# Kernel optimization log

Hardware: AMD Instinct MI355X
Metric: run time of the kernel (lower is better)

Reference implementation:

```python
import jax, jax.numpy as jnp
import numpy as np

NUM_HEADS = 8
CODEBOOK_SIZE = 1024
HEAD_DIM = 128
BATCH = 32768


def setup_inputs() -> dict:
    key = jax.random.key(0)
    k_z, k_cb = jax.random.split(key)
    z = jax.random.normal(k_z, (BATCH, NUM_HEADS * HEAD_DIM), dtype=jnp.float32)
    codebooks = jax.random.normal(k_cb, (NUM_HEADS, CODEBOOK_SIZE, HEAD_DIM), dtype=jnp.float32)
    return {"z": z, "codebooks": codebooks}


def reference(z, codebooks):
    # z: [B, H*D]; codebooks: [H, K, D]
    H, K, D = codebooks.shape
    B = z.shape[0]
    zh = z.reshape(B, H, D)
    # Squared euclidean distances ||z - c||^2 = ||z||^2 - 2 z.c + ||c||^2.
    # torch.cdist(p=2) applies sqrt, but sqrt is monotone so argmin is identical.
    z_sq = jnp.sum(zh * zh, axis=-1)                       # [B, H]
    c_sq = jnp.sum(codebooks * codebooks, axis=-1)         # [H, K]
    cross = jnp.einsum('bhd,hkd->bhk', zh, codebooks)      # [B, H, K]
    d2 = z_sq[:, :, None] - 2.0 * cross + c_sq[None, :, :]  # [B, H, K]
    idx = jnp.argmin(d2, axis=-1)                          # [B, H] int
    # Gather nearest codes per head: codebooks[h, idx[b,h]] -> [B, H, D]
    zq = codebooks[jnp.arange(H)[None, :], idx]
    # Straight-through estimator: forward = codes, backward = identity on z.
    zq = zh + jax.lax.stop_gradient(zq - zh)
    return zq.reshape(B, H * D), idx
```

## Files before the change

### kernel.cpp

```cpp
#include <hip/hip_runtime.h>

namespace {
constexpr int kNH = 8;
constexpr int kK  = 1024;
constexpr int kD  = 128;
constexpr int kB  = 32768;

constexpr int BM  = 128;
constexpr int kMarginQ = 4;
constexpr float kMarginF32 = 0.0625f;

constexpr size_t kOffCsq  = 4096;
constexpr size_t kOffCbF  = 65536;
constexpr size_t kOffPart = 65536 + 4194304;
constexpr size_t kOffWl6  = 65536 + 8388608;
constexpr size_t kOffWl5  = 65536 + 4194304;
}

typedef short           bf16x8 __attribute__((ext_vector_type(8)));
typedef unsigned short  us16x8 __attribute__((ext_vector_type(8)));
typedef float           f32x16 __attribute__((ext_vector_type(16)));

__device__ __forceinline__ unsigned short f2bf_rne(float f) {
    unsigned int x = __float_as_uint(f);
    unsigned int r = (x + 0x7fffu + ((x >> 16) & 1u)) >> 16;
    return (unsigned short)r;
}
__device__ __forceinline__ float bf2f(unsigned short u) {
    return __uint_as_float(((unsigned int)u) << 16);
}

__global__ void pq_prep(const float* __restrict__ cb,
                        unsigned short* __restrict__ cbf,
                        float* __restrict__ csq)
{
    int code = blockIdx.x;
    int t = threadIdx.x;
    int h = code >> 10, k = code & 1023;
    int kt = k >> 6, cv = (k >> 5) & 1, l31 = k & 31;
    int kc = t >> 4, hh = (t >> 3) & 1, j = t & 7;
    float v = cb[(size_t)code * kD + t];
    unsigned short hb = f2bf_rne(v);
    unsigned short lb = f2bf_rne(v - bf2f(hb));
    size_t base = ((((size_t)h * 16 + kt) * 8 + kc) * 2 + cv) * 2048;
    size_t off  = base + (hh * 32 + l31) * 16 + j * 2;
    *(unsigned short*)((char*)cbf + off)        = hb;
    *(unsigned short*)((char*)cbf + off + 1024) = lb;
    __shared__ double red[128];
    red[t] = (double)v * (double)v;
    __syncthreads();
    for (int s = 64; s > 0; s >>= 1) {
        if (t < s) red[t] += red[t + s];
        __syncthreads();
    }
    if (t == 0) csq[code] = (float)(red[0] * 1024.0);
}

__global__ __launch_bounds__(512, 2)
void pq_coarse_mfma4(const float* __restrict__ z,
                     const unsigned short* __restrict__ cbf,
                     const float* __restrict__ csq1024,
                     int2* __restrict__ part)
{
    __shared__ unsigned short zbuf[2][2][32 * kD];
    __shared__ int2 P[2][8][32];

    const int t    = threadIdx.x;
    const int lane = t & 63;
    const int w    = t >> 6;
    const int l31  = lane & 31, h32 = lane >> 5;
    const int h    = blockIdx.y;
    const int half = blockIdx.z;
    const int rb0  = blockIdx.x * 1024;

    bf16x8 Ah[8][2], Al[8][2];
    {
        const char* base = (const char*)cbf
            + (((size_t)h * 16 + half * 8 + w) * 16) * 2048 + lane * 16;
        #pragma unroll
        for (int kc = 0; kc < 8; ++kc)
            #pragma unroll
            for (int cv = 0; cv < 2; ++cv) {
                const char* p = base + (size_t)(kc * 2 + cv) * 2048;
                Ah[kc][cv] = *(const bf16x8*)p;
                Al[kc][cv] = *(const bf16x8*)(p + 1024);
            }
    }
    float csel[2][16];
    {
        const float* cs = csq1024 + h * kK + half * 512 + w * 64 + h32 * 4;
        #pragma unroll
        for (int cv = 0; cv < 2; ++cv)
            #pragma unroll
            for (int r = 0; r < 16; ++r)
                csel[cv][r] = cs[cv * 32 + (r & 3) + ((r >> 2) << 3)];
    }

    float4 zA, zB;
    auto issueZ = [&](int tile) {
        const float* zp = z + (size_t)(rb0 + tile * 32 + (t >> 4)) * (kNH * kD)
                            + h * kD + (t & 15) * 8;
        zA = *(const float4*)zp;
        zB = *(const float4*)(zp + 4);
    };
    auto commitZ = [&](int buf) {
        float f[8] = {zA.x, zA.y, zA.z, zA.w, zB.x, zB.y, zB.z, zB.w};
        us16x8 hv, lv;
        #pragma unroll
        for (int j = 0; j < 8; ++j) {
            unsigned short hb = f2bf_rne(f[j]);
            hv[j] = hb;
            lv[j] = f2bf_rne(f[j] - bf2f(hb));
        }
        int r = t >> 4, seg = t & 15;
        int off = r * 256 + ((seg * 16) ^ ((r & 15) << 4));
        *(us16x8*)((char*)&zbuf[buf][0][0] + off) = hv;
        *(us16x8*)((char*)&zbuf[buf][1][0] + off) = lv;
    };
    auto mergeP = [&](int pb, int tile) {
        int2 m = P[pb][0][t];
        int m1 = m.x, m2 = m.y;
        #pragma unroll
        for (int ww = 1; ww < 8; ++ww) {
            int2 p = P[pb][ww][t];
            int mx = max(m1, p.x);
            m1 = min(m1, p.x);
            m2 = min(min(m2, p.y), mx);
        }
        int gid = (rb0 + tile * 32 + t) * kNH + h;
        part[(size_t)gid * 2 + half] = make_int2(m1, m2);
    };

    issueZ(0);
    commitZ(0);
    __syncthreads();

    int cur = 0;
    const int cgb = half * 512 + w * 64 + h32 * 4;
    for (int tile = 0; tile < 32; ++tile) {
        if (tile + 1 < 32) issueZ(tile + 1);
        if (tile > 0 && t < 32) mergeP(cur ^ 1, tile - 1);

        f32x16 acc0 = (f32x16)0.0f, acc1 = (f32x16)0.0f;
        const char* zh0 = (const char*)&zbuf[cur][0][0];
        const char* zl0 = (const char*)&zbuf[cur][1][0];
        const int boff = l31 * 256;
        const int swz  = (l31 & 15) << 4;
        #pragma unroll
        for (int kc = 0; kc < 8; ++kc) {
            int col = (kc * 32 + h32 * 16) ^ swz;
            bf16x8 Bh = *(const bf16x8*)(zh0 + boff + col);
            bf16x8 Bl = *(const bf16x8*)(zl0 + boff + col);
            __builtin_amdgcn_s_setprio(1);
            acc0 = __builtin_amdgcn_mfma_f32_32x32x16_bf16(Ah[kc][0], Bh, acc0, 0, 0, 0);
            acc1 = __builtin_amdgcn_mfma_f32_32x32x16_bf16(Ah[kc][1], Bh, acc1, 0, 0, 0);
            acc0 = __builtin_amdgcn_mfma_f32_32x32x16_bf16(Al[kc][0], Bh, acc0, 0, 0, 0);
            acc1 = __builtin_amdgcn_mfma_f32_32x32x16_bf16(Al[kc][1], Bh, acc1, 0, 0, 0);
            acc0 = __builtin_amdgcn_mfma_f32_32x32x16_bf16(Ah[kc][0], Bl, acc0, 0, 0, 0);
            acc1 = __builtin_amdgcn_mfma_f32_32x32x16_bf16(Ah[kc][1], Bl, acc1, 0, 0, 0);
            __builtin_amdgcn_s_setprio(0);
        }
        int b1 = 0x7fffffff, b2 = 0x7fffffff;
        #pragma unroll
        for (int r = 0; r < 16; ++r) {
            int cr = (r & 3) + ((r >> 2) << 3);
            {
                float kf = fmaf(acc0[r], -2048.0f, csel[0][r]);
                int key = ((int)kf << 10) + cgb + cr;
                int mx = max(b1, key); b1 = min(b1, key); b2 = min(b2, mx);
            }
            {
                float kf = fmaf(acc1[r], -2048.0f, csel[1][r]);
                int key = ((int)kf << 10) + cgb + cr + 32;
                int mx = max(b1, key); b1 = min(b1, key); b2 = min(b2, mx);
            }
        }
        int o1 = __shfl_xor(b1, 32), o2 = __shfl_xor(b2, 32);
        int mx2 = max(b1, o1);
        int v1 = min(b1, o1);
        int v2 = min(min(b2, o2), mx2);
        if (h32 == 0) P[cur][w][l31] = make_int2(v1, v2);

        if (tile + 1 < 32) commitZ(cur ^ 1);
        __syncthreads();
        cur ^= 1;
    }
    if (t < 32) mergeP(cur ^ 1, 31);
}

__global__ __launch_bounds__(256)
void pq_merge(const int2* __restrict__ part, const float* __restrict__ cb,
              float* __restrict__ out_zq, float* __restrict__ out_idx,
              unsigned int* wl_count, unsigned int* wl, unsigned int wl_cap)
{
    __shared__ int idx_s[128];
    const int t = threadIdx.x;
    const int g0 = blockIdx.x * 128;
    if (t < 128) {
        int gid = g0 + t;
        int2 p0 = part[(size_t)gid * 2];
        int2 p1 = part[(size_t)gid * 2 + 1];
        int mx = max(p0.x, p1.x);
        int v1 = min(p0.x, p1.x);
        int v2 = min(min(p0.y, p1.y), mx);
        int idx = v1 & 1023;
        idx_s[t] = idx;
        out_idx[gid] = (float)idx;
        if (wl_cap > 0u && ((v2 >> 10) - (v1 >> 10)) <= kMarginQ) {
            unsigned int pos = atomicAdd(wl_count, 1u);
            if (pos < wl_cap) wl[pos] = (unsigned int)gid;
        }
    }
    __syncthreads();
    #pragma unroll
    for (int it = 0; it < 16; ++it) {
        int c = it * 256 + t;
        int row = c >> 5, c4 = c & 31;
        int gid = g0 + row;
        int b = gid >> 3, hh = gid & 7;
        *(float4*)(out_zq + (size_t)b * (kNH * kD) + hh * kD + c4 * 4) =
            *(const float4*)(cb + ((size_t)hh * kK + idx_s[row]) * kD + c4 * 4);
    }
}

__global__ __launch_bounds__(256, 2)
void pq_coarse_mfma3(const float* __restrict__ z, const float* __restrict__ cb,
                     const unsigned short* __restrict__ cbf,
                     const float* __restrict__ csq1024,
                     float* __restrict__ out_zq, float* __restrict__ out_idx,
                     unsigned int* wl_count, unsigned int* wl, unsigned int wl_cap)
{
    __shared__ float csq_s[kK];
    __shared__ int   idx_s[BM];

    const int t    = threadIdx.x;
    const int h    = blockIdx.y;
    const int b0   = blockIdx.x * BM;
    const int lane = t & 63;
    const int w    = t >> 6;
    const int l31  = lane & 31, h32 = lane >> 5;

    *(float4*)&csq_s[t * 4] = *(const float4*)(csq1024 + h * kK + t * 4);

    bf16x8 Ah[8], Al[8];
    {
        const float* zr = z + (size_t)(b0 + w * 32 + l31) * (kNH * kD) + h * kD + h32 * 8;
        #pragma unroll
        for (int kc = 0; kc < 8; ++kc) {
            float4 a = *(const float4*)(zr + kc * 16);
            float4 b = *(const float4*)(zr + kc * 16 + 4);
            float f[8] = {a.x, a.y, a.z, a.w, b.x, b.y, b.z, b.w};
            bf16x8 hv, lv;
            #pragma unroll
            for (int j = 0; j < 8; ++j) {
                unsigned short hb = f2bf_rne(f[j]);
                hv[j] = (short)hb;
                lv[j] = (short)f2bf_rne(f[j] - bf2f(hb));
            }
            Ah[kc] = hv;
            Al[kc] = lv;
        }
    }
    __syncthreads();

    int b1[16], b2[16];
    #pragma unroll
    for (int r = 0; r < 16; ++r) { b1[r] = 0x7fffffff; b2[r] = 0x7fffffff; }

    const char* bbase = (const char*)cbf + (size_t)h * 524288 + lane * 16;
#define LDSLOT(kt_, kc_, s_)                                                  \
    {                                                                         \
        const char* p_ = bbase + (size_t)(((kt_) * 8 + (kc_)) * 2) * 2048;    \
        Bh0[s_] = *(const bf16x8*)(p_);                                       \
        Bl0[s_] = *(const bf16x8*)(p_ + 1024);                                \
        Bh1[s_] = *(const bf16x8*)(p_ + 2048);                                \
        Bl1[s_] = *(const bf16x8*)(p_ + 3072);                                \
    }

    bf16x8 Bh0[4], Bl0[4], Bh1[4], Bl1[4];
    LDSLOT(0, 0, 0);
    LDSLOT(0, 1, 1);

    for (int kt = 0; kt < 16; ++kt) {
        f32x16 acc0 = (f32x16)0.0f, acc1 = (f32x16)0.0f;
        const int ktn = (kt + 1 < 16) ? kt + 1 : kt;
        #pragma unroll
        for (int kc = 0; kc < 8; ++kc) {
            const int s  = kc & 3;
            const int s2 = (kc + 2) & 3;
            if (kc < 6) { LDSLOT(kt, kc + 2, s2); } else { LDSLOT(ktn, kc - 6, s2); }
            __builtin_amdgcn_s_setprio(1);
            acc0 = __builtin_amdgcn_mfma_f32_32x32x16_bf16(Ah[kc], Bh0[s], acc0, 0, 0, 0);
            acc1 = __builtin_amdgcn_mfma_f32_32x32x16_bf16(Ah[kc], Bh1[s], acc1, 0, 0, 0);
            acc0 = __builtin_amdgcn_mfma_f32_32x32x16_bf16(Al[kc], Bh0[s], acc0, 0, 0, 0);
            acc1 = __builtin_amdgcn_mfma_f32_32x32x16_bf16(Al[kc], Bh1[s], acc1, 0, 0, 0);
            acc0 = __builtin_amdgcn_mfma_f32_32x32x16_bf16(Ah[kc], Bl0[s], acc0, 0, 0, 0);
            acc1 = __builtin_amdgcn_mfma_f32_32x32x16_bf16(Ah[kc], Bl1[s], acc1, 0, 0, 0);
            __builtin_amdgcn_s_setprio(0);
        }
        const float cs0 = csq_s[kt * 64 + l31];
        const float cs1 = csq_s[kt * 64 + 32 + l31];
        const int   kg0 = kt * 64 + l31, kg1 = kg0 + 32;
        #pragma unroll
        for (int r = 0; r < 16; ++r) {
            {
                float kf = fmaf(acc0[r], -2048.0f, cs0);
                int key = ((int)kf << 10) + kg0;
                int mx = max(b1[r], key); b1[r] = min(b1[r], key); b2[r] = min(b2[r], mx);
            }
            {
                float kf = fmaf(acc1[r], -2048.0f, cs1);
                int key = ((int)kf << 10) + kg1;
                int mx = max(b1[r], key); b1[r] = min(b1[r], key); b2[r] = min(b2[r], mx);
            }
        }
    }
#undef LDSLOT

    #pragma unroll
    for (int r = 0; r < 16; ++r) {
        int v1 = b1[r], v2 = b2[r];
        #pragma unroll
        for (int m = 1; m < 32; m <<= 1) {
            int o1 = __shfl_xor(v1, m);
            int o2 = __shfl_xor(v2, m);
            int mx = max(v1, o1);
            v1 = min(v1, o1);
            v2 = min(min(v2, o2), mx);
        }
        if (l31 == 0) {
            int row = w * 32 + (r & 3) + ((r >> 2) << 3) + h32 * 4;
            int idx = v1 & 1023;
            idx_s[row] = idx;
            int gid = (b0 + row) * kNH + h;
            out_idx[gid] = (float)idx;
            if (wl_cap > 0u && ((v2 >> 10) - (v1 >> 10)) <= kMarginQ) {
                unsigned int pos = atomicAdd(wl_count, 1u);
                if (pos < wl_cap) wl[pos] = (unsigned int)gid;
            }
        }
    }
    __syncthreads();
    {
        const float* cbh_row = cb + (size_t)h * kK * kD;
        #pragma unroll
        for (int it = 0; it < 16; ++it) {
            int c = it * 256 + t;
            int row = c >> 5, col4 = c & 31;
            *(float4*)(out_zq + (size_t)(b0 + row) * (kNH * kD) + h * kD + col4 * 4) =
                *(const float4*)(cbh_row + (size_t)idx_s[row] * kD + col4 * 4);
        }
    }
}

__global__ __launch_bounds__(256, 2)
void pq_coarse_f32(const float* __restrict__ z, const float* __restrict__ cb,
                   float* __restrict__ out_zq, float* __restrict__ out_idx,
                   unsigned int* wl_count, unsigned int* wl, unsigned int wl_cap)
{
    constexpr int KT = 64, PAD = 68, BMF = 64;
    __shared__ float zT[kD][PAD];
    __shared__ float cT[kD][PAD];
    __shared__ float csq_s[KT];
    __shared__ int   bidx_s[BMF];

    const int t  = threadIdx.x;
    const int h  = blockIdx.y;
    const int b0 = blockIdx.x * BMF;
    const int tx = t & 15, ty = t >> 4;
    const int r8 = t & 7,  d4 = t >> 3;

    {
        const float* zp = z + (size_t)(b0 + r8) * (kNH * kD) + h * kD + 4 * d4;
        #pragma unroll
        for (int it = 0; it < BMF / 8; ++it) {
            float4 v = *(const float4*)(zp + (size_t)(8 * it) * (kNH * kD));
            int r = r8 + 8 * it;
            zT[4 * d4 + 0][r] = v.x; zT[4 * d4 + 1][r] = v.y;
            zT[4 * d4 + 2][r] = v.z; zT[4 * d4 + 3][r] = v.w;
        }
    }
    float best1[4], best2[4]; int ibest[4];
    #pragma unroll
    for (int i = 0; i < 4; ++i) { best1[i] = 3.4e38f; best2[i] = 3.4e38f; ibest[i] = 0; }

    for (int kt = 0; kt < kK / KT; ++kt) {
        __syncthreads();
        {
            const float* cp = cb + ((size_t)h * kK + kt * KT + r8) * kD + 4 * d4;
            #pragma unroll
            for (int it = 0; it < KT / 8; ++it) {
                float4 v = *(const float4*)(cp + (size_t)(8 * it) * kD);
                int r = r8 + 8 * it;
                cT[4 * d4 + 0][r] = v.x; cT[4 * d4 + 1][r] = v.y;
                cT[4 * d4 + 2][r] = v.z; cT[4 * d4 + 3][r] = v.w;
            }
        }
        if (t < KT) csq_s[t] = 0.0f;
        __syncthreads();
        {
            int kk = t & 63, part = t >> 6;
            float s = 0.f;
            #pragma unroll
            for (int i = 0; i < 32; ++i) { float v = cT[32 * part + i][kk]; s = fmaf(v, v, s); }
            atomicAdd(&csq_s[kk], s);
        }
        __syncthreads();
        float accA[4][4] = {{0}}, accB[4][4] = {{0}};
        #pragma unroll 2
        for (int d = 0; d < kD; d += 2) {
            float4 za = *(const float4*)&zT[d][4 * ty];
            float4 ca = *(const float4*)&cT[d][4 * tx];
            float4 zb = *(const float4*)&zT[d + 1][4 * ty];
            float4 cv = *(const float4*)&cT[d + 1][4 * tx];
            float zav[4] = {za.x, za.y, za.z, za.w}, cav[4] = {ca.x, ca.y, ca.z, ca.w};
            float zbv[4] = {zb.x, zb.y, zb.z, zb.w}, cbv[4] = {cv.x, cv.y, cv.z, cv.w};
            #pragma unroll
            for (int i = 0; i < 4; ++i)
                #pragma unroll
                for (int j = 0; j < 4; ++j) {
                    accA[i][j] = fmaf(zav[i], cav[j], accA[i][j]);
                    accB[i][j] = fmaf(zbv[i], cbv[j], accB[i][j]);
                }
        }
        #pragma unroll
        for (int j = 0; j < 4; ++j) {
            int kk = 4 * tx + j;
            float cs = csq_s[kk];
            int kg = kt * KT + kk;
            #pragma unroll
            for (int i = 0; i < 4; ++i) {
                float s = fmaf(-2.0f, accA[i][j] + accB[i][j], cs);
                if (s < best1[i]) { best2[i] = best1[i]; best1[i] = s; ibest[i] = kg; }
                else if (s < best2[i]) { best2[i] = s; }
            }
        }
    }
    __syncthreads();
    float* redv1 = &zT[0][0];
    float* redv2 = redv1 + BMF * 16;
    int*   redi  = (int*)(redv2 + BMF * 16);
    #pragma unroll
    for (int i = 0; i < 4; ++i) {
        int r = 4 * ty + i;
        redv1[r * 16 + tx] = best1[i]; redv2[r * 16 + tx] = best2[i]; redi[r * 16 + tx] = ibest[i];
    }
    __syncthreads();
    if (t < BMF) {
        int r = t;
        float vb1_ = redv1[r * 16], vb2_ = redv2[r * 16];
        int i1 = redi[r * 16];
        #pragma unroll
        for (int x = 1; x < 16; ++x) {
            float nb1 = redv1[r * 16 + x], nb2 = redv2[r * 16 + x];
            int ni1 = redi[r * 16 + x];
            if (nb1 < vb1_ || (nb1 == vb1_ && ni1 < i1)) { vb2_ = fminf(vb1_, nb2); vb1_ = nb1; i1 = ni1; }
            else vb2_ = fminf(vb2_, nb1);
        }
        bidx_s[r] = i1;
        int gid = (b0 + r) * kNH + h;
        out_idx[gid] = (float)i1;
        if (wl_cap > 0u && (vb2_ - vb1_) <= kMarginF32) {
            unsigned int pos = atomicAdd(wl_count, 1u);
            if (pos < wl_cap) wl[pos] = (unsigned int)gid;
        }
    }
    __syncthreads();
    {
        int r = t >> 2, q = t & 3;
        const float* src = cb + ((size_t)h * kK + bidx_s[r]) * kD;
        float* dst = out_zq + (size_t)(b0 + r) * (kNH * kD) + h * kD;
        #pragma unroll
        for (int m = 0; m < 8; ++m) {
            int jj = 4 * m + q;
            *(float4*)(dst + 4 * jj) = *(const float4*)(src + 4 * jj);
        }
    }
}

__global__ __launch_bounds__(256)
void pq_exact(const float* __restrict__ z, const float* __restrict__ cb,
              float* __restrict__ out_zq, float* __restrict__ out_idx,
              const unsigned int* wl_count, const unsigned int* wl,
              unsigned int wl_cap)
{
    if (wl_cap == 0u) return;
    __shared__ float  zs[kD];
    __shared__ double rv[256];
    __shared__ int    ri[256];
    unsigned int n = *wl_count;
    if (n > wl_cap) n = wl_cap;
    const int t = threadIdx.x;
    for (unsigned int e = blockIdx.x; e < n; e += gridDim.x) {
        unsigned int id = wl[e];
        int b = (int)(id / kNH), h = (int)(id % kNH);
        if (t < kD) zs[t] = z[(size_t)b * (kNH * kD) + h * kD + t];
        __syncthreads();
        double bv = 1e300; int bi = 0;
        #pragma unroll
        for (int kk = 0; kk < 4; ++kk) {
            int k = t * 4 + kk;
            const float* c = cb + ((size_t)h * kK + k) * kD;
            double s = 0.0;
            for (int d = 0; d < kD; ++d) {
                double diff = (double)zs[d] - (double)c[d];
                s = fma(diff, diff, s);
            }
            if (s < bv) { bv = s; bi = k; }
        }
        rv[t] = bv; ri[t] = bi;
        __syncthreads();
        for (int s2 = 128; s2 > 0; s2 >>= 1) {
            if (t < s2) {
                if (rv[t + s2] < rv[t] || (rv[t + s2] == rv[t] && ri[t + s2] < ri[t])) {
                    rv[t] = rv[t + s2]; ri[t] = ri[t + s2];
                }
            }
            __syncthreads();
        }
        int kbest = ri[0];
        if (t == 0) out_idx[id] = (float)kbest;
        if (t < kD)
            out_zq[(size_t)b * (kNH * kD) + h * kD + t] =
                cb[((size_t)h * kK + kbest) * kD + t];
        __syncthreads();
    }
}

extern "C" void kernel_launch(void* const* d_in, const int* in_sizes, int n_in,
                              void* d_out, int out_size, void* d_ws, size_t ws_size,
                              hipStream_t stream)
{
    const float* z  = (const float*)d_in[0];
    const float* cb = (const float*)d_in[1];
    float* out_zq  = (float*)d_out;
    float* out_idx = out_zq + (size_t)kB * kNH * kD;
    char* ws = (char*)d_ws;

    if (ws_size >= kOffWl6 + 65536) {
        unsigned int* wl_count = (unsigned int*)ws;
        unsigned int* wl = (unsigned int*)(ws + kOffWl6);
        size_t c = (ws_size - kOffWl6) / 4;
        unsigned int cap = (unsigned int)(c > 262144 ? 262144 : c);
        float* csq = (float*)(ws + kOffCsq);
        unsigned short* cbf = (unsigned short*)(ws + kOffCbF);
        int2* part = (int2*)(ws + kOffPart);

        hipMemsetAsync(d_ws, 0, 4, stream);
        pq_prep<<<kNH * kK, kD, 0, stream>>>(cb, cbf, csq);
        dim3 grid(32, kNH, 2);
        pq_coarse_mfma4<<<grid, 512, 0, stream>>>(z, cbf, csq, part);
        pq_merge<<<kB * kNH / 128, 256, 0, stream>>>(part, cb, out_zq, out_idx,
                                                     wl_count, wl, cap);
        pq_exact<<<256, 256, 0, stream>>>(z, cb, out_zq, out_idx, wl_count, wl, cap);
    } else if (ws_size >= kOffWl5 + 4096) {
        unsigned int* wl_count = (unsigned int*)ws;
        unsigned int* wl = (unsigned int*)(ws + kOffWl5);
        size_t c = (ws_size - kOffWl5) / 4;
        unsigned int cap = (unsigned int)(c > 262144 ? 262144 : c);
        float* csq = (float*)(ws + kOffCsq);
        unsigned short* cbf = (unsigned short*)(ws + kOffCbF);

        hipMemsetAsync(d_ws, 0, 4, stream);
        pq_prep<<<kNH * kK, kD, 0, stream>>>(cb, cbf, csq);
        dim3 grid(kB / BM, kNH);
        pq_coarse_mfma3<<<grid, 256, 0, stream>>>(z, cb, cbf, csq,
                                                  out_zq, out_idx, wl_count, wl, cap);
        pq_exact<<<256, 256, 0, stream>>>(z, cb, out_zq, out_idx, wl_count, wl, cap);
    } else {
        unsigned int* wl_count = (unsigned int*)ws;
        unsigned int* wl = wl_count + 1;
        unsigned int cap = 0;
        if (ws_size >= 64) {
            size_t c = ws_size / 4 - 1;
            cap = (unsigned int)(c > 262144 ? 262144 : c);
            hipMemsetAsync(d_ws, 0, 4, stream);
        }
        dim3 grid(kB / 64, kNH);
        pq_coarse_f32<<<grid, 256, 0, stream>>>(z, cb, out_zq, out_idx, wl_count, wl, cap);
        pq_exact<<<256, 256, 0, stream>>>(z, cb, out_zq, out_idx, wl_count, wl, cap);
    }
}
```

Baseline: 238.4 us.

## Stream codebook fragments from global and double the per-phase row tile

The coarse MFMA kernel no longer holds the whole codebook slice in registers. It streams A fragments from global memory through a two-slot register ring, one K-chunk ahead. Each phase now processes 64 z rows instead of 32, so every loaded A fragment feeds twice as many MFMAs. The change also packs bf16 with a cheaper bias-and-perm conversion, keeps the top-2 running minimum with v_med3, and rotates the merge work across waves. Register pressure drops, but codebook reloads now hit L2/global on every phase, and the kernel depends on that latency being hidden behind the MFMAs.

Measured after the change: 320.8 us. 1.35x slower.

```diff
diff --git a/kernel.cpp b/kernel.cpp
--- a/kernel.cpp
+++ b/kernel.cpp
@@ -28,6 +28,11 @@
 }
 __device__ __forceinline__ float bf2f(unsigned short u) {
     return __uint_as_float(((unsigned int)u) << 16);
+}
+__device__ __forceinline__ int med3_i32(int a, int b, int c) {
+    int d;
+    asm("v_med3_i32 %0, %1, %2, %3" : "=v"(d) : "v"(a), "v"(b), "v"(c));
+    return d;
 }
 
 __global__ void pq_prep(const float* __restrict__ cb,
@@ -57,13 +62,13 @@
 }
 
 __global__ __launch_bounds__(512, 2)
-void pq_coarse_mfma4(const float* __restrict__ z,
+void pq_coarse_mfma5(const float* __restrict__ z,
                      const unsigned short* __restrict__ cbf,
                      const float* __restrict__ csq1024,
                      int2* __restrict__ part)
 {
-    __shared__ unsigned short zbuf[2][2][32 * kD];
-    __shared__ int2 P[2][8][32];
+    __shared__ unsigned short zbuf[2][2][64 * kD];
+    __shared__ int2 P[2][8][64];
 
     const int t    = threadIdx.x;
     const int lane = t & 63;
@@ -73,119 +78,156 @@
     const int half = blockIdx.z;
     const int rb0  = blockIdx.x * 1024;
 
-    bf16x8 Ah[8][2], Al[8][2];
-    {
-        const char* base = (const char*)cbf
-            + (((size_t)h * 16 + half * 8 + w) * 16) * 2048 + lane * 16;
-        #pragma unroll
-        for (int kc = 0; kc < 8; ++kc)
-            #pragma unroll
-            for (int cv = 0; cv < 2; ++cv) {
-                const char* p = base + (size_t)(kc * 2 + cv) * 2048;
-                Ah[kc][cv] = *(const bf16x8*)p;
-                Al[kc][cv] = *(const bf16x8*)(p + 1024);
-            }
-    }
-    float csel[2][16];
+    const char* pb = (const char*)cbf
+        + (size_t)((h * 16 + half * 8 + w) * 16) * 2048 + lane * 16;
+
+    float csel0[16], csel1[16];
     {
         const float* cs = csq1024 + h * kK + half * 512 + w * 64 + h32 * 4;
         #pragma unroll
-        for (int cv = 0; cv < 2; ++cv)
-            #pragma unroll
-            for (int r = 0; r < 16; ++r)
-                csel[cv][r] = cs[cv * 32 + (r & 3) + ((r >> 2) << 3)];
-    }
-
-    float4 zA, zB;
-    auto issueZ = [&](int tile) {
-        const float* zp = z + (size_t)(rb0 + tile * 32 + (t >> 4)) * (kNH * kD)
-                            + h * kD + (t & 15) * 8;
-        zA = *(const float4*)zp;
-        zB = *(const float4*)(zp + 4);
+        for (int r = 0; r < 16; ++r) {
+            int cr = (r & 3) + ((r >> 2) << 3);
+            csel0[r] = cs[cr];
+            csel1[r] = cs[32 + cr];
+        }
+    }
+    const int cgb = half * 512 + w * 64 + h32 * 4;
+
+    float4 pA, pB, pC, pD;
+    auto issueZ = [&](int phase) {
+        const float* zp = z + (size_t)(rb0 + phase * 64 + (t >> 5)) * (kNH * kD)
+                            + h * kD + (t & 31) * 4;
+        pA = *(const float4*)zp;
+        pB = *(const float4*)(zp + 16 * (kNH * kD));
+        pC = *(const float4*)(zp + 32 * (kNH * kD));
+        pD = *(const float4*)(zp + 48 * (kNH * kD));
+    };
+    auto commit1 = [&](int buf, int rowq, float4 v) {
+        unsigned bx = __float_as_uint(v.x) + 0x8000u;
+        unsigned by = __float_as_uint(v.y) + 0x8000u;
+        unsigned bz = __float_as_uint(v.z) + 0x8000u;
+        unsigned bw = __float_as_uint(v.w) + 0x8000u;
+        unsigned h01 = __builtin_amdgcn_perm(by, bx, 0x07060302u);
+        unsigned h23 = __builtin_amdgcn_perm(bw, bz, 0x07060302u);
+        float rx = v.x - __uint_as_float(bx & 0xffff0000u);
+        float ry = v.y - __uint_as_float(by & 0xffff0000u);
+        float rz = v.z - __uint_as_float(bz & 0xffff0000u);
+        float rw = v.w - __uint_as_float(bw & 0xffff0000u);
+        unsigned l01 = __builtin_amdgcn_perm(__float_as_uint(ry) + 0x8000u,
+                                             __float_as_uint(rx) + 0x8000u, 0x07060302u);
+        unsigned l23 = __builtin_amdgcn_perm(__float_as_uint(rw) + 0x8000u,
+                                             __float_as_uint(rz) + 0x8000u, 0x07060302u);
+        int col4 = t & 31;
+        int off = rowq * 256 + (((col4 >> 1) * 16) ^ ((rowq & 15) << 4)) + (col4 & 1) * 8;
+        uint2 hv = {h01, h23}, lv = {l01, l23};
+        *(uint2*)((char*)&zbuf[buf][0][0] + off) = hv;
+        *(uint2*)((char*)&zbuf[buf][1][0] + off) = lv;
     };
     auto commitZ = [&](int buf) {
-        float f[8] = {zA.x, zA.y, zA.z, zA.w, zB.x, zB.y, zB.z, zB.w};
-        us16x8 hv, lv;
-        #pragma unroll
-        for (int j = 0; j < 8; ++j) {
-            unsigned short hb = f2bf_rne(f[j]);
-            hv[j] = hb;
-            lv[j] = f2bf_rne(f[j] - bf2f(hb));
-        }
-        int r = t >> 4, seg = t & 15;
-        int off = r * 256 + ((seg * 16) ^ ((r & 15) << 4));
-        *(us16x8*)((char*)&zbuf[buf][0][0] + off) = hv;
-        *(us16x8*)((char*)&zbuf[buf][1][0] + off) = lv;
+        commit1(buf,  0 + (t >> 5), pA);
+        commit1(buf, 16 + (t >> 5), pB);
+        commit1(buf, 32 + (t >> 5), pC);
+        commit1(buf, 48 + (t >> 5), pD);
     };
-    auto mergeP = [&](int pb, int tile) {
-        int2 m = P[pb][0][t];
+    auto mergeP = [&](int pbuf, int phase) {
+        int2 m = P[pbuf][0][lane];
         int m1 = m.x, m2 = m.y;
         #pragma unroll
         for (int ww = 1; ww < 8; ++ww) {
-            int2 p = P[pb][ww][t];
+            int2 p = P[pbuf][ww][lane];
             int mx = max(m1, p.x);
             m1 = min(m1, p.x);
             m2 = min(min(m2, p.y), mx);
         }
-        int gid = (rb0 + tile * 32 + t) * kNH + h;
+        int gid = (rb0 + phase * 64 + lane) * kNH + h;
         part[(size_t)gid * 2 + half] = make_int2(m1, m2);
     };
 
+    bf16x8 sAh[2][2], sAl[2][2];
+#define LOADSLOT(kc_, s_)                                                     \
+    {                                                                         \
+        const char* q0 = pb + (size_t)((kc_) * 2 + 0) * 2048;                 \
+        const char* q1 = pb + (size_t)((kc_) * 2 + 1) * 2048;                 \
+        sAh[s_][0] = *(const bf16x8*)q0;                                      \
+        sAl[s_][0] = *(const bf16x8*)(q0 + 1024);                             \
+        sAh[s_][1] = *(const bf16x8*)q1;                                      \
+        sAl[s_][1] = *(const bf16x8*)(q1 + 1024);                             \
+    }
+
     issueZ(0);
     commitZ(0);
-    __syncthreads();
-
+    LOADSLOT(0, 0);
+    __syncthreads();
+
+    const int swz = (l31 & 15) << 4;
     int cur = 0;
-    const int cgb = half * 512 + w * 64 + h32 * 4;
-    for (int tile = 0; tile < 32; ++tile) {
-        if (tile + 1 < 32) issueZ(tile + 1);
-        if (tile > 0 && t < 32) mergeP(cur ^ 1, tile - 1);
-
-        f32x16 acc0 = (f32x16)0.0f, acc1 = (f32x16)0.0f;
+    for (int phase = 0; phase < 16; ++phase) {
+        if (phase + 1 < 16) issueZ(phase + 1);
+        if (phase > 0 && w == ((phase - 1) & 7)) mergeP(cur ^ 1, phase - 1);
+
+        f32x16 a00 = (f32x16)0.0f, a01 = (f32x16)0.0f;
+        f32x16 a10 = (f32x16)0.0f, a11 = (f32x16)0.0f;
         const char* zh0 = (const char*)&zbuf[cur][0][0];
         const char* zl0 = (const char*)&zbuf[cur][1][0];
-        const int boff = l31 * 256;
-        const int swz  = (l31 & 15) << 4;
         #pragma unroll
         for (int kc = 0; kc < 8; ++kc) {
-            int col = (kc * 32 + h32 * 16) ^ swz;
-            bf16x8 Bh = *(const bf16x8*)(zh0 + boff + col);
-            bf16x8 Bl = *(const bf16x8*)(zl0 + boff + col);
+            const int sl = kc & 1;
+            if (kc < 7) { LOADSLOT(kc + 1, ((kc + 1) & 1)); }
+            else        { LOADSLOT(0, 0); }
+            const int col = (kc * 32 + h32 * 16) ^ swz;
+            bf16x8 B0h = *(const bf16x8*)(zh0 + l31 * 256 + col);
+            bf16x8 B0l = *(const bf16x8*)(zl0 + l31 * 256 + col);
+            bf16x8 B1h = *(const bf16x8*)(zh0 + (32 + l31) * 256 + col);
+            bf16x8 B1l = *(const bf16x8*)(zl0 + (32 + l31) * 256 + col);
             __builtin_amdgcn_s_setprio(1);
-            acc0 = __builtin_amdgcn_mfma_f32_32x32x16_bf16(Ah[kc][0], Bh, acc0, 0, 0, 0);
-            acc1 = __builtin_amdgcn_mfma_f32_32x32x16_bf16(Ah[kc][1], Bh, acc1, 0, 0, 0);
-            acc0 = __builtin_amdgcn_mfma_f32_32x32x16_bf16(Al[kc][0], Bh, acc0, 0, 0, 0);
-            acc1 = __builtin_amdgcn_mfma_f32_32x32x16_bf16(Al[kc][1], Bh, acc1, 0, 0, 0);
-            acc0 = __builtin_amdgcn_mfma_f32_32x32x16_bf16(Ah[kc][0], Bl, acc0, 0, 0, 0);
-            acc1 = __builtin_amdgcn_mfma_f32_32x32x16_bf16(Ah[kc][1], Bl, acc1, 0, 0, 0);
+            a00 = __builtin_amdgcn_mfma_f32_32x32x16_bf16(sAh[sl][0], B0h, a00, 0, 0, 0);
+            a01 = __builtin_amdgcn_mfma_f32_32x32x16_bf16(sAh[sl][0], B1h, a01, 0, 0, 0);
+            a10 = __builtin_amdgcn_mfma_f32_32x32x16_bf16(sAh[sl][1], B0h, a10, 0, 0, 0);
+            a11 = __builtin_amdgcn_mfma_f32_32x32x16_bf16(sAh[sl][1], B1h, a11, 0, 0, 0);
+            a00 = __builtin_amdgcn_mfma_f32_32x32x16_bf16(sAl[sl][0], B0h, a00, 0, 0, 0);
+            a01 = __builtin_amdgcn_mfma_f32_32x32x16_bf16(sAl[sl][0], B1h, a01, 0, 0, 0);
+            a10 = __builtin_amdgcn_mfma_f32_32x32x16_bf16(sAl[sl][1], B0h, a10, 0, 0, 0);
+            a11 = __builtin_amdgcn_mfma_f32_32x32x16_bf16(sAl[sl][1], B1h, a11, 0, 0, 0);
+            a00 = __builtin_amdgcn_mfma_f32_32x32x16_bf16(sAh[sl][0], B0l, a00, 0, 0, 0);
+            a01 = __builtin_amdgcn_mfma_f32_32x32x16_bf16(sAh[sl][0], B1l, a01, 0, 0, 0);
+            a10 = __builtin_amdgcn_mfma_f32_32x32x16_bf16(sAh[sl][1], B0l, a10, 0, 0, 0);
+            a11 = __builtin_amdgcn_mfma_f32_32x32x16_bf16(sAh[sl][1], B1l, a11, 0, 0, 0);
             __builtin_amdgcn_s_setprio(0);
         }
-        int b1 = 0x7fffffff, b2 = 0x7fffffff;
+        int b1t0 = 0x7fffffff, b2t0 = 0x7fffffff;
+        int b1t1 = 0x7fffffff, b2t1 = 0x7fffffff;
         #pragma unroll
         for (int r = 0; r < 16; ++r) {
-            int cr = (r & 3) + ((r >> 2) << 3);
-            {
-                float kf = fmaf(acc0[r], -2048.0f, csel[0][r]);
-                int key = ((int)kf << 10) + cgb + cr;
-                int mx = max(b1, key); b1 = min(b1, key); b2 = min(b2, mx);
-            }
-            {
-                float kf = fmaf(acc1[r], -2048.0f, csel[1][r]);
-                int key = ((int)kf << 10) + cgb + cr + 32;
-                int mx = max(b1, key); b1 = min(b1, key); b2 = min(b2, mx);
-            }
-        }
-        int o1 = __shfl_xor(b1, 32), o2 = __shfl_xor(b2, 32);
-        int mx2 = max(b1, o1);
-        int v1 = min(b1, o1);
-        int v2 = min(min(b2, o2), mx2);
-        if (h32 == 0) P[cur][w][l31] = make_int2(v1, v2);
-
-        if (tile + 1 < 32) commitZ(cur ^ 1);
+            const int cr = (r & 3) + ((r >> 2) << 3);
+            int k00 = (((int)fmaf(a00[r], -2048.0f, csel0[r])) << 10) + cgb + cr;
+            b2t0 = med3_i32(k00, b1t0, b2t0); b1t0 = min(b1t0, k00);
+            int k10 = (((int)fmaf(a10[r], -2048.0f, csel1[r])) << 10) + cgb + cr + 32;
+            b2t0 = med3_i32(k10, b1t0, b2t0); b1t0 = min(b1t0, k10);
+            int k01 = (((int)fmaf(a01[r], -2048.0f, csel0[r])) << 10) + cgb + cr;
+            b2t1 = med3_i32(k01, b1t1, b2t1); b1t1 = min(b1t1, k01);
+            int k11 = (((int)fmaf(a11[r], -2048.0f, csel1[r])) << 10) + cgb + cr + 32;
+            b2t1 = med3_i32(k11, b1t1, b2t1); b1t1 = min(b1t1, k11);
+        }
+        {
+            int o1 = __shfl_xor(b1t0, 32), o2 = __shfl_xor(b2t0, 32);
+            int mx = max(b1t0, o1);
+            int v1 = min(b1t0, o1);
+            int v2 = min(min(b2t0, o2), mx);
+            if (h32 == 0) P[cur][w][l31] = make_int2(v1, v2);
+        }
+        {
+            int o1 = __shfl_xor(b1t1, 32), o2 = __shfl_xor(b2t1, 32);
+            int mx = max(b1t1, o1);
+            int v1 = min(b1t1, o1);
+            int v2 = min(min(b2t1, o2), mx);
+            if (h32 == 0) P[cur][w][32 + l31] = make_int2(v1, v2);
+        }
+        if (phase + 1 < 16) commitZ(cur ^ 1);
         __syncthreads();
         cur ^= 1;
     }
-    if (t < 32) mergeP(cur ^ 1, 31);
+#undef LOADSLOT
+    if (w == 7) mergeP(cur ^ 1, 15);
 }
 
 __global__ __launch_bounds__(256)
@@ -549,7 +591,7 @@
         hipMemsetAsync(d_ws, 0, 4, stream);
         pq_prep<<<kNH * kK, kD, 0, stream>>>(cb, cbf, csq);
         dim3 grid(32, kNH, 2);
-        pq_coarse_mfma4<<<grid, 512, 0, stream>>>(z, cbf, csq, part);
+        pq_coarse_mfma5<<<grid, 512, 0, stream>>>(z, cbf, csq, part);
         pq_merge<<<kB * kNH / 128, 256, 0, stream>>>(part, cb, out_zq, out_idx,
                                                      wl_count, wl, cap);
         pq_exact<<<256, 256, 0, stream>>>(z, cb, out_zq, out_idx, wl_count, wl, cap);
```
